# Performance work log

Measured on AMD Instinct MI355X. Metric: run time of the kernel, lower is better.

The kernel has to match this reference:

```python
import jax, jax.numpy as jnp
import numpy as np

B, T, D = 4, 2048, 1024
H = 16
DH = D // H
BASE = 10000.0


def _rope_tables(seq_len, dim):
    inv_freq = 1.0 / (BASE ** (np.arange(0, dim, 2, dtype=np.float32) / dim))
    pos = np.arange(seq_len, dtype=np.float32)
    freqs = np.outer(pos, inv_freq)            # (T, dim/2)
    emb = np.concatenate([freqs, freqs], -1)   # (T, dim)
    return jnp.asarray(np.cos(emb)), jnp.asarray(np.sin(emb))


def setup_inputs() -> dict:
    key = jax.random.key(0)
    ks = jax.random.split(key, 5)
    s = 1.0 / np.sqrt(D)
    x = jax.random.normal(ks[0], (B, T, D), jnp.float32)
    Wqkv = jax.random.normal(ks[1], (D, 3 * D), jnp.float32) * s
    bqkv = jnp.zeros((3 * D,), jnp.float32)
    Wproj = jax.random.normal(ks[2], (D, D), jnp.float32) * s
    bproj = jnp.zeros((D,), jnp.float32)
    cos, sin = _rope_tables(T, DH)
    return {"x": x, "Wqkv": Wqkv, "bqkv": bqkv, "Wproj": Wproj,
            "bproj": bproj, "cos": cos, "sin": sin}


def _rotate_half(u):
    u1, u2 = jnp.split(u, 2, axis=-1)
    return jnp.concatenate([-u2, u1], axis=-1)


def reference(x, Wqkv, bqkv, Wproj, bproj, cos, sin):
    b, t, d = x.shape
    qkv = x @ Wqkv + bqkv                       # (B, T, 3D)
    qkv = qkv.reshape(b, t, 3, H, DH)           # matches '(three h d)' order
    q, k, v = qkv[:, :, 0], qkv[:, :, 1], qkv[:, :, 2]  # (B, T, H, DH)
    c = cos[None, :, None, :]                   # (1, T, 1, DH)
    s = sin[None, :, None, :]
    q = q * c + _rotate_half(q) * s
    k = k * c + _rotate_half(k) * s
    scale = DH ** -0.5
    attn = jnp.einsum('bthd,bshd->bhts', q, k) * scale   # (B, H, T, T)
    attn = jax.nn.softmax(attn, axis=-1)
    out = jnp.einsum('bhts,bshd->bthd', attn, v)          # (B, T, H, DH)
    out = out.reshape(b, t, d)
    return out @ Wproj + bproj
```

## Files before the change

### kernel.cpp

```cpp
#include <hip/hip_runtime.h>


typedef _Float16 half_t;
typedef _Float16 half8 __attribute__((ext_vector_type(8)));
typedef _Float16 half4v __attribute__((ext_vector_type(4)));
typedef float floatx4 __attribute__((ext_vector_type(4)));

#define MFMA_F16 __builtin_amdgcn_mfma_f32_16x16x32_f16

constexpr int Bdim = 4, T = 2048, D = 1024, H = 16, DH = 64;
constexpr int Mrows = Bdim * T;
constexpr int N1 = 3 * D;
constexpr int KD = D;

constexpr float QSCALE = 0.125f * 1.4426950408889634f;
constexpr float CSHIFT = 4.0f * 1.4426950408889634f;

__global__ __launch_bounds__(256) void cvt_kernel(const float* __restrict__ s,
                                                  half_t* __restrict__ d, int n4) {
  int i = blockIdx.x * 256 + threadIdx.x;
  if (i < n4) {
    float4 v = ((const float4*)s)[i];
    half4v h;
    h[0] = (half_t)v.x; h[1] = (half_t)v.y; h[2] = (half_t)v.z; h[3] = (half_t)v.w;
    ((half4v*)d)[i] = h;
  }
}

__global__ __launch_bounds__(64) void cvt_transpose(const float* __restrict__ W,
                                                    half_t* __restrict__ Wt,
                                                    int Kr, int Nc) {
  __shared__ half_t Th[32][36];
  const int l = threadIdx.x;
  const int n0 = blockIdx.x * 32, k0 = blockIdx.y * 32;
#pragma unroll
  for (int i = 0; i < 4; ++i) {
    int kk = (l >> 3) + i * 8;
    int nn4 = (l & 7) * 4;
    float4 v = *(const float4*)(W + (size_t)(k0 + kk) * Nc + n0 + nn4);
    half4v h;
    h[0] = (half_t)v.x; h[1] = (half_t)v.y; h[2] = (half_t)v.z; h[3] = (half_t)v.w;
    *(half4v*)&Th[kk][nn4] = h;
  }
  __syncthreads();
#pragma unroll
  for (int i = 0; i < 4; ++i) {
    int nn = (l >> 3) + i * 8;
    int kk4 = (l & 7) * 4;
    half4v h;
#pragma unroll
    for (int j = 0; j < 4; ++j) h[j] = Th[kk4 + j][nn];
    *(half4v*)(Wt + (size_t)(n0 + nn) * Kr + k0 + kk4) = h;
  }
}

__global__ __launch_bounds__(256) void gemm_qkv_rope(
    const half_t* __restrict__ X, const half_t* __restrict__ Wt,
    const float* __restrict__ bias, const float* __restrict__ cosT,
    const float* __restrict__ sinT,
    half_t* __restrict__ Q, half_t* __restrict__ K, half_t* __restrict__ V) {
  __shared__ half_t As[128][40];
  __shared__ half_t Bs[128][40];
  const int tid = threadIdx.x;
  const int lane = tid & 63, wv = tid >> 6;
  const int wm = wv >> 1, wn = wv & 1;
  const int qd = lane >> 4, ln = lane & 15;
  const int bn = blockIdx.x, bm = blockIdx.y;

  floatx4 acc[4][4] = {};

  for (int k0 = 0; k0 < KD; k0 += 32) {
#pragma unroll
    for (int p = 0; p < 2; ++p) {
      int c = tid + p * 256;
      int row = c >> 2, col = (c & 3) << 3;
      *(half8*)&As[row][col] =
          *(const half8*)(X + (size_t)(bm * 128 + row) * KD + k0 + col);
      *(half8*)&Bs[row][col] =
          *(const half8*)(Wt + (size_t)(bn * 128 + row) * KD + k0 + col);
    }
    __syncthreads();

    half8 af[4], bf[4];
#pragma unroll
    for (int mi = 0; mi < 4; ++mi)
      af[mi] = *(const half8*)&As[wm * 64 + mi * 16 + ln][qd * 8];
#pragma unroll
    for (int ni = 0; ni < 4; ++ni)
      bf[ni] = *(const half8*)&Bs[wn * 64 + ni * 16 + ln][qd * 8];
#pragma unroll
    for (int mi = 0; mi < 4; ++mi)
#pragma unroll
      for (int ni = 0; ni < 4; ++ni)
        acc[mi][ni] = MFMA_F16(af[mi], bf[ni], acc[mi][ni], 0, 0, 0);
    __syncthreads();
  }

  const int n0 = bn * 128 + wn * 64;
  const int sreg = n0 >> 10;
  const int h = (n0 & 1023) >> 6;
  half_t* OUT = (sreg == 0) ? Q : (sreg == 1) ? K : V;
  const float qscale = (sreg == 0) ? QSCALE : 1.0f;
  float bv[4];
#pragma unroll
  for (int ni = 0; ni < 4; ++ni) bv[ni] = bias[n0 + ni * 16 + ln];

#pragma unroll
  for (int mi = 0; mi < 4; ++mi) {
#pragma unroll
    for (int r = 0; r < 4; ++r) {
      int m = bm * 128 + wm * 64 + mi * 16 + qd * 4 + r;
      int b = m >> 11, t = m & (T - 1);
      float v0 = acc[mi][0][r] + bv[0];
      float v1 = acc[mi][1][r] + bv[1];
      float v2 = acc[mi][2][r] + bv[2];
      float v3 = acc[mi][3][r] + bv[3];
      float o0, o1, o2, o3;
      if (sreg < 2) {
        float c0 = cosT[t * 64 + ln],      s0 = sinT[t * 64 + ln];
        float c1 = cosT[t * 64 + 16 + ln], s1 = sinT[t * 64 + 16 + ln];
        float c2 = cosT[t * 64 + 32 + ln], s2 = sinT[t * 64 + 32 + ln];
        float c3 = cosT[t * 64 + 48 + ln], s3 = sinT[t * 64 + 48 + ln];
        o0 = v0 * c0 - v2 * s0;
        o1 = v1 * c1 - v3 * s1;
        o2 = v2 * c2 + v0 * s2;
        o3 = v3 * c3 + v1 * s3;
      } else {
        o0 = v0; o1 = v1; o2 = v2; o3 = v3;
      }
      size_t base = ((size_t)(b * H + h) * T + t) * DH;
      OUT[base + 0 * 16 + ln] = (half_t)(o0 * qscale);
      OUT[base + 1 * 16 + ln] = (half_t)(o1 * qscale);
      OUT[base + 2 * 16 + ln] = (half_t)(o2 * qscale);
      OUT[base + 3 * 16 + ln] = (half_t)(o3 * qscale);
    }
  }
}

__global__ __launch_bounds__(256, 4) void flash_attn(
    const half_t* __restrict__ Q, const half_t* __restrict__ K,
    const half_t* __restrict__ V, half_t* __restrict__ AO) {
  __shared__ half_t Klds[64][72];
  __shared__ half_t Vt[64][72];
  __shared__ half_t Plds[4][32][72];
  const int tid = threadIdx.x;
  const int lane = tid & 63, wv = tid >> 6;
  const int qd = lane >> 4, ln = lane & 15;
  const int bh = blockIdx.y;
  const int q0 = blockIdx.x * 128 + wv * 32;
  const half_t* Qb = Q + (size_t)bh * T * DH;
  const half_t* Kb = K + (size_t)bh * T * DH;
  const half_t* Vb = V + (size_t)bh * T * DH;

  half8 qf[2][2];
#pragma unroll
  for (int mi = 0; mi < 2; ++mi)
#pragma unroll
    for (int ks = 0; ks < 2; ++ks)
      qf[mi][ks] = *(const half8*)(Qb + (size_t)(q0 + mi * 16 + ln) * DH + ks * 32 + qd * 8);

  floatx4 Oacc[2][4] = {};
  floatx4 Lacc[2] = {};
  half8 ones;
#pragma unroll
  for (int j = 0; j < 8; ++j) ones[j] = (half_t)1.0f;

  const int pswz = (ln >> 2) & 3;

  for (int s0 = 0; s0 < T; s0 += 64) {
#pragma unroll
    for (int p = 0; p < 2; ++p) {
      int c = tid + p * 256;
      int s = c & 63, dh0 = (c >> 6) << 3;
      *(half8*)&Klds[s][dh0] = *(const half8*)(Kb + (size_t)(s0 + s) * DH + dh0);
      half8 vv = *(const half8*)(Vb + (size_t)(s0 + s) * DH + dh0);
#pragma unroll
      for (int i = 0; i < 8; ++i) Vt[dh0 + i][s] = vv[i];
    }
    __syncthreads();

    floatx4 sacc[2][4] = {};
#pragma unroll
    for (int ks = 0; ks < 2; ++ks)
#pragma unroll
      for (int ni = 0; ni < 4; ++ni) {
        half8 kf = *(const half8*)&Klds[ni * 16 + ln][ks * 32 + qd * 8];
#pragma unroll
        for (int mi = 0; mi < 2; ++mi)
          sacc[mi][ni] = MFMA_F16(qf[mi][ks], kf, sacc[mi][ni], 0, 0, 0);
      }

#pragma unroll
    for (int mi = 0; mi < 2; ++mi)
#pragma unroll
      for (int ni = 0; ni < 4; ++ni) {
        int colw = ((((ni * 2) + (ln >> 3)) ^ qd) << 3) | (ln & 7);
#pragma unroll
        for (int r = 0; r < 4; ++r) {
          float p = __builtin_amdgcn_exp2f(sacc[mi][ni][r] - CSHIFT);
          Plds[wv][mi * 16 + qd * 4 + r][colw] = (half_t)p;
        }
      }

#pragma unroll
    for (int ks = 0; ks < 2; ++ks) {
      half8 pf[2];
#pragma unroll
      for (int mi = 0; mi < 2; ++mi)
        pf[mi] = *(const half8*)&Plds[wv][mi * 16 + ln][((ks * 4 + qd) ^ pswz) << 3];
#pragma unroll
      for (int ni = 0; ni < 4; ++ni) {
        half8 vf = *(const half8*)&Vt[ni * 16 + ln][ks * 32 + qd * 8];
#pragma unroll
        for (int mi = 0; mi < 2; ++mi)
          Oacc[mi][ni] = MFMA_F16(pf[mi], vf, Oacc[mi][ni], 0, 0, 0);
      }
#pragma unroll
      for (int mi = 0; mi < 2; ++mi)
        Lacc[mi] = MFMA_F16(pf[mi], ones, Lacc[mi], 0, 0, 0);
    }
    __syncthreads();
  }

  const int b = bh >> 4, h = bh & 15;
#pragma unroll
  for (int mi = 0; mi < 2; ++mi) {
#pragma unroll
    for (int r = 0; r < 4; ++r) {
      float invL = 1.f / Lacc[mi][r];
      int t = q0 + mi * 16 + qd * 4 + r;
      size_t base = ((size_t)b * T + t) * D + h * DH;
#pragma unroll
      for (int ni = 0; ni < 4; ++ni)
        AO[base + ni * 16 + ln] = (half_t)(Oacc[mi][ni][r] * invL);
    }
  }
}

__global__ __launch_bounds__(256) void gemm_proj(
    const half_t* __restrict__ X, const half_t* __restrict__ Wt,
    const float* __restrict__ bias, float* __restrict__ OUTF) {
  __shared__ half_t As[128][40];
  __shared__ half_t Bs[128][40];
  const int tid = threadIdx.x;
  const int lane = tid & 63, wv = tid >> 6;
  const int wm = wv >> 1, wn = wv & 1;
  const int qd = lane >> 4, ln = lane & 15;
  const int bn = blockIdx.x, bm = blockIdx.y;

  floatx4 acc[4][4] = {};

  for (int k0 = 0; k0 < KD; k0 += 32) {
#pragma unroll
    for (int p = 0; p < 2; ++p) {
      int c = tid + p * 256;
      int row = c >> 2, col = (c & 3) << 3;
      *(half8*)&As[row][col] =
          *(const half8*)(X + (size_t)(bm * 128 + row) * KD + k0 + col);
      *(half8*)&Bs[row][col] =
          *(const half8*)(Wt + (size_t)(bn * 128 + row) * KD + k0 + col);
    }
    __syncthreads();

    half8 af[4], bf[4];
#pragma unroll
    for (int mi = 0; mi < 4; ++mi)
      af[mi] = *(const half8*)&As[wm * 64 + mi * 16 + ln][qd * 8];
#pragma unroll
    for (int ni = 0; ni < 4; ++ni)
      bf[ni] = *(const half8*)&Bs[wn * 64 + ni * 16 + ln][qd * 8];
#pragma unroll
    for (int mi = 0; mi < 4; ++mi)
#pragma unroll
      for (int ni = 0; ni < 4; ++ni)
        acc[mi][ni] = MFMA_F16(af[mi], bf[ni], acc[mi][ni], 0, 0, 0);
    __syncthreads();
  }

  const int n0 = bn * 128 + wn * 64;
  float bv[4];
#pragma unroll
  for (int ni = 0; ni < 4; ++ni) bv[ni] = bias[n0 + ni * 16 + ln];
#pragma unroll
  for (int mi = 0; mi < 4; ++mi) {
#pragma unroll
    for (int r = 0; r < 4; ++r) {
      int m = bm * 128 + wm * 64 + mi * 16 + qd * 4 + r;
#pragma unroll
      for (int ni = 0; ni < 4; ++ni)
        OUTF[(size_t)m * D + n0 + ni * 16 + ln] = acc[mi][ni][r] + bv[ni];
    }
  }
}

extern "C" void kernel_launch(void* const* d_in, const int* in_sizes, int n_in,
                              void* d_out, int out_size, void* d_ws, size_t ws_size,
                              hipStream_t stream) {
  const float* x     = (const float*)d_in[0];
  const float* Wqkv  = (const float*)d_in[1];
  const float* bqkv  = (const float*)d_in[2];
  const float* Wproj = (const float*)d_in[3];
  const float* bproj = (const float*)d_in[4];
  const float* cosT  = (const float*)d_in[5];
  const float* sinT  = (const float*)d_in[6];
  float* out = (float*)d_out;

  half_t* xh      = (half_t*)d_ws;
  half_t* Wqkvt   = xh + (size_t)Mrows * KD;
  half_t* Wprojt  = Wqkvt + (size_t)KD * N1;
  half_t* Qb      = Wprojt + (size_t)D * D;
  half_t* Kb      = Qb + (size_t)Bdim * H * T * DH;
  half_t* Vb      = Kb + (size_t)Bdim * H * T * DH;
  half_t* AO      = xh;

  cvt_kernel<<<(Mrows * KD / 4 + 255) / 256, 256, 0, stream>>>(x, xh, Mrows * KD / 4);
  cvt_transpose<<<dim3(N1 / 32, KD / 32), 64, 0, stream>>>(Wqkv, Wqkvt, KD, N1);
  cvt_transpose<<<dim3(D / 32, KD / 32), 64, 0, stream>>>(Wproj, Wprojt, KD, D);

  gemm_qkv_rope<<<dim3(N1 / 128, Mrows / 128), 256, 0, stream>>>(
      xh, Wqkvt, bqkv, cosT, sinT, Qb, Kb, Vb);
  flash_attn<<<dim3(T / 128, Bdim * H), 256, 0, stream>>>(Qb, Kb, Vb, AO);
  gemm_proj<<<dim3(D / 128, Mrows / 128), 256, 0, stream>>>(AO, Wprojt, bproj, out);
}
```

Measured before the change: 332.5 us.

## Transpose V in QKV epilogue, keep P in registers, use direct global-to-LDS loads

The QKV GEMM epilogue now writes V pre-transposed (head-dim major), so the attention kernel no longer does a scalar LDS transpose of V. Attention computes S^T via swapped MFMA operands so probabilities stay in registers and feed 16x16x16 MFMAs directly, which removes the P round-trip through LDS and the ones-MFMA row sum. Row sums are now accumulated in registers and reduced with shuffles. Both GEMMs switch to global_load_lds direct loads into unpadded LDS tiles, which drops the register staging but may add bank conflicts on the fragment reads. The occupancy hint of 4 on the attention kernel is also removed.

```diff
diff --git a/kernel.cpp b/kernel.cpp
--- a/kernel.cpp
+++ b/kernel.cpp
@@ -7,6 +7,7 @@
 typedef float floatx4 __attribute__((ext_vector_type(4)));
 
 #define MFMA_F16 __builtin_amdgcn_mfma_f32_16x16x32_f16
+#define MFMA16   __builtin_amdgcn_mfma_f32_16x16x16f16
 
 constexpr int Bdim = 4, T = 2048, D = 1024, H = 16, DH = 64;
 constexpr int Mrows = Bdim * T;
@@ -15,6 +16,12 @@
 
 constexpr float QSCALE = 0.125f * 1.4426950408889634f;
 constexpr float CSHIFT = 4.0f * 1.4426950408889634f;
+
+__device__ __forceinline__ void gl_lds16(const half_t* g, half_t* l) {
+  __builtin_amdgcn_global_load_lds(
+      (const __attribute__((address_space(1))) void*)g,
+      (__attribute__((address_space(3))) void*)l, 16, 0, 0);
+}
 
 __global__ __launch_bounds__(256) void cvt_kernel(const float* __restrict__ s,
                                                   half_t* __restrict__ d, int n4) {
@@ -59,8 +66,8 @@
     const float* __restrict__ bias, const float* __restrict__ cosT,
     const float* __restrict__ sinT,
     half_t* __restrict__ Q, half_t* __restrict__ K, half_t* __restrict__ V) {
-  __shared__ half_t As[128][40];
-  __shared__ half_t Bs[128][40];
+  __shared__ half_t As[128 * 32];
+  __shared__ half_t Bs[128 * 32];
   const int tid = threadIdx.x;
   const int lane = tid & 63, wv = tid >> 6;
   const int wm = wv >> 1, wn = wv & 1;
@@ -74,20 +81,18 @@
     for (int p = 0; p < 2; ++p) {
       int c = tid + p * 256;
       int row = c >> 2, col = (c & 3) << 3;
-      *(half8*)&As[row][col] =
-          *(const half8*)(X + (size_t)(bm * 128 + row) * KD + k0 + col);
-      *(half8*)&Bs[row][col] =
-          *(const half8*)(Wt + (size_t)(bn * 128 + row) * KD + k0 + col);
+      gl_lds16(X + (size_t)(bm * 128 + row) * KD + k0 + col, As + c * 8);
+      gl_lds16(Wt + (size_t)(bn * 128 + row) * KD + k0 + col, Bs + c * 8);
     }
     __syncthreads();
 
     half8 af[4], bf[4];
 #pragma unroll
     for (int mi = 0; mi < 4; ++mi)
-      af[mi] = *(const half8*)&As[wm * 64 + mi * 16 + ln][qd * 8];
+      af[mi] = *(const half8*)&As[(wm * 64 + mi * 16 + ln) * 32 + qd * 8];
 #pragma unroll
     for (int ni = 0; ni < 4; ++ni)
-      bf[ni] = *(const half8*)&Bs[wn * 64 + ni * 16 + ln][qd * 8];
+      bf[ni] = *(const half8*)&Bs[(wn * 64 + ni * 16 + ln) * 32 + qd * 8];
 #pragma unroll
     for (int mi = 0; mi < 4; ++mi)
 #pragma unroll
@@ -99,50 +104,60 @@
   const int n0 = bn * 128 + wn * 64;
   const int sreg = n0 >> 10;
   const int h = (n0 & 1023) >> 6;
-  half_t* OUT = (sreg == 0) ? Q : (sreg == 1) ? K : V;
-  const float qscale = (sreg == 0) ? QSCALE : 1.0f;
   float bv[4];
 #pragma unroll
   for (int ni = 0; ni < 4; ++ni) bv[ni] = bias[n0 + ni * 16 + ln];
 
-#pragma unroll
-  for (int mi = 0; mi < 4; ++mi) {
-#pragma unroll
-    for (int r = 0; r < 4; ++r) {
-      int m = bm * 128 + wm * 64 + mi * 16 + qd * 4 + r;
-      int b = m >> 11, t = m & (T - 1);
-      float v0 = acc[mi][0][r] + bv[0];
-      float v1 = acc[mi][1][r] + bv[1];
-      float v2 = acc[mi][2][r] + bv[2];
-      float v3 = acc[mi][3][r] + bv[3];
-      float o0, o1, o2, o3;
-      if (sreg < 2) {
+  if (sreg == 2) {
+#pragma unroll
+    for (int mi = 0; mi < 4; ++mi) {
+      int m0 = bm * 128 + wm * 64 + mi * 16 + qd * 4;
+      int b = m0 >> 11, t0 = m0 & (T - 1);
+#pragma unroll
+      for (int ni = 0; ni < 4; ++ni) {
+        int dh = ni * 16 + ln;
+        half4v hv;
+#pragma unroll
+        for (int r = 0; r < 4; ++r) hv[r] = (half_t)(acc[mi][ni][r] + bv[ni]);
+        *(half4v*)(V + ((size_t)(b * H + h) * DH + dh) * T + t0) = hv;
+      }
+    }
+  } else {
+    const float qscale = (sreg == 0) ? QSCALE : 1.0f;
+    half_t* OUT = (sreg == 0) ? Q : K;
+#pragma unroll
+    for (int mi = 0; mi < 4; ++mi) {
+#pragma unroll
+      for (int r = 0; r < 4; ++r) {
+        int m = bm * 128 + wm * 64 + mi * 16 + qd * 4 + r;
+        int b = m >> 11, t = m & (T - 1);
+        float v0 = acc[mi][0][r] + bv[0];
+        float v1 = acc[mi][1][r] + bv[1];
+        float v2 = acc[mi][2][r] + bv[2];
+        float v3 = acc[mi][3][r] + bv[3];
         float c0 = cosT[t * 64 + ln],      s0 = sinT[t * 64 + ln];
         float c1 = cosT[t * 64 + 16 + ln], s1 = sinT[t * 64 + 16 + ln];
         float c2 = cosT[t * 64 + 32 + ln], s2 = sinT[t * 64 + 32 + ln];
         float c3 = cosT[t * 64 + 48 + ln], s3 = sinT[t * 64 + 48 + ln];
-        o0 = v0 * c0 - v2 * s0;
-        o1 = v1 * c1 - v3 * s1;
-        o2 = v2 * c2 + v0 * s2;
-        o3 = v3 * c3 + v1 * s3;
-      } else {
-        o0 = v0; o1 = v1; o2 = v2; o3 = v3;
-      }
-      size_t base = ((size_t)(b * H + h) * T + t) * DH;
-      OUT[base + 0 * 16 + ln] = (half_t)(o0 * qscale);
-      OUT[base + 1 * 16 + ln] = (half_t)(o1 * qscale);
-      OUT[base + 2 * 16 + ln] = (half_t)(o2 * qscale);
-      OUT[base + 3 * 16 + ln] = (half_t)(o3 * qscale);
-    }
-  }
-}
-
-__global__ __launch_bounds__(256, 4) void flash_attn(
+        float o0 = v0 * c0 - v2 * s0;
+        float o1 = v1 * c1 - v3 * s1;
+        float o2 = v2 * c2 + v0 * s2;
+        float o3 = v3 * c3 + v1 * s3;
+        size_t base = ((size_t)(b * H + h) * T + t) * DH;
+        OUT[base + 0 * 16 + ln] = (half_t)(o0 * qscale);
+        OUT[base + 1 * 16 + ln] = (half_t)(o1 * qscale);
+        OUT[base + 2 * 16 + ln] = (half_t)(o2 * qscale);
+        OUT[base + 3 * 16 + ln] = (half_t)(o3 * qscale);
+      }
+    }
+  }
+}
+
+__global__ __launch_bounds__(256) void flash_attn(
     const half_t* __restrict__ Q, const half_t* __restrict__ K,
-    const half_t* __restrict__ V, half_t* __restrict__ AO) {
+    const half_t* __restrict__ Vt, half_t* __restrict__ AO) {
   __shared__ half_t Klds[64][72];
-  __shared__ half_t Vt[64][72];
-  __shared__ half_t Plds[4][32][72];
+  __shared__ half_t Vlds[64][72];
   const int tid = threadIdx.x;
   const int lane = tid & 63, wv = tid >> 6;
   const int qd = lane >> 4, ln = lane & 15;
@@ -150,7 +165,7 @@
   const int q0 = blockIdx.x * 128 + wv * 32;
   const half_t* Qb = Q + (size_t)bh * T * DH;
   const half_t* Kb = K + (size_t)bh * T * DH;
-  const half_t* Vb = V + (size_t)bh * T * DH;
+  const half_t* Vb = Vt + (size_t)bh * DH * T;
 
   half8 qf[2][2];
 #pragma unroll
@@ -160,26 +175,19 @@
       qf[mi][ks] = *(const half8*)(Qb + (size_t)(q0 + mi * 16 + ln) * DH + ks * 32 + qd * 8);
 
   floatx4 Oacc[2][4] = {};
-  floatx4 Lacc[2] = {};
-  half8 ones;
-#pragma unroll
-  for (int j = 0; j < 8; ++j) ones[j] = (half_t)1.0f;
-
-  const int pswz = (ln >> 2) & 3;
+  float Ls[2] = {0.f, 0.f};
 
   for (int s0 = 0; s0 < T; s0 += 64) {
 #pragma unroll
     for (int p = 0; p < 2; ++p) {
-      int c = tid + p * 256;
-      int s = c & 63, dh0 = (c >> 6) << 3;
-      *(half8*)&Klds[s][dh0] = *(const half8*)(Kb + (size_t)(s0 + s) * DH + dh0);
-      half8 vv = *(const half8*)(Vb + (size_t)(s0 + s) * DH + dh0);
-#pragma unroll
-      for (int i = 0; i < 8; ++i) Vt[dh0 + i][s] = vv[i];
-    }
-    __syncthreads();
-
-    floatx4 sacc[2][4] = {};
+      int idx = tid + p * 256;
+      int r = idx >> 3, ch = (idx & 7) << 3;
+      *(half8*)&Klds[r][ch] = *(const half8*)(Kb + (size_t)(s0 + r) * DH + ch);
+      *(half8*)&Vlds[r][ch] = *(const half8*)(Vb + (size_t)r * T + s0 + ch);
+    }
+    __syncthreads();
+
+    floatx4 sacc[4][2] = {};
 #pragma unroll
     for (int ks = 0; ks < 2; ++ks)
 #pragma unroll
@@ -187,39 +195,39 @@
         half8 kf = *(const half8*)&Klds[ni * 16 + ln][ks * 32 + qd * 8];
 #pragma unroll
         for (int mi = 0; mi < 2; ++mi)
-          sacc[mi][ni] = MFMA_F16(qf[mi][ks], kf, sacc[mi][ni], 0, 0, 0);
-      }
-
-#pragma unroll
-    for (int mi = 0; mi < 2; ++mi)
-#pragma unroll
-      for (int ni = 0; ni < 4; ++ni) {
-        int colw = ((((ni * 2) + (ln >> 3)) ^ qd) << 3) | (ln & 7);
-#pragma unroll
-        for (int r = 0; r < 4; ++r) {
-          float p = __builtin_amdgcn_exp2f(sacc[mi][ni][r] - CSHIFT);
-          Plds[wv][mi * 16 + qd * 4 + r][colw] = (half_t)p;
-        }
-      }
-
-#pragma unroll
-    for (int ks = 0; ks < 2; ++ks) {
-      half8 pf[2];
-#pragma unroll
-      for (int mi = 0; mi < 2; ++mi)
-        pf[mi] = *(const half8*)&Plds[wv][mi * 16 + ln][((ks * 4 + qd) ^ pswz) << 3];
-#pragma unroll
-      for (int ni = 0; ni < 4; ++ni) {
-        half8 vf = *(const half8*)&Vt[ni * 16 + ln][ks * 32 + qd * 8];
+          sacc[ni][mi] = MFMA_F16(kf, qf[mi][ks], sacc[ni][mi], 0, 0, 0);
+      }
+
+    half4v pf[2][4];
+#pragma unroll
+    for (int ni = 0; ni < 4; ++ni)
+#pragma unroll
+      for (int mi = 0; mi < 2; ++mi) {
+        float p0 = __builtin_amdgcn_exp2f(sacc[ni][mi][0] - CSHIFT);
+        float p1 = __builtin_amdgcn_exp2f(sacc[ni][mi][1] - CSHIFT);
+        float p2 = __builtin_amdgcn_exp2f(sacc[ni][mi][2] - CSHIFT);
+        float p3 = __builtin_amdgcn_exp2f(sacc[ni][mi][3] - CSHIFT);
+        Ls[mi] += (p0 + p1) + (p2 + p3);
+        half4v h; h[0] = (half_t)p0; h[1] = (half_t)p1; h[2] = (half_t)p2; h[3] = (half_t)p3;
+        pf[mi][ni] = h;
+      }
+
+#pragma unroll
+    for (int ni = 0; ni < 4; ++ni)
+#pragma unroll
+      for (int di = 0; di < 4; ++di) {
+        half4v vf = *(const half4v*)&Vlds[di * 16 + ln][ni * 16 + qd * 4];
 #pragma unroll
         for (int mi = 0; mi < 2; ++mi)
-          Oacc[mi][ni] = MFMA_F16(pf[mi], vf, Oacc[mi][ni], 0, 0, 0);
-      }
-#pragma unroll
-      for (int mi = 0; mi < 2; ++mi)
-        Lacc[mi] = MFMA_F16(pf[mi], ones, Lacc[mi], 0, 0, 0);
-    }
-    __syncthreads();
+          Oacc[mi][di] = MFMA16(pf[mi][ni], vf, Oacc[mi][di], 0, 0, 0);
+      }
+    __syncthreads();
+  }
+
+#pragma unroll
+  for (int mi = 0; mi < 2; ++mi) {
+    Ls[mi] += __shfl_xor(Ls[mi], 16);
+    Ls[mi] += __shfl_xor(Ls[mi], 32);
   }
 
   const int b = bh >> 4, h = bh & 15;
@@ -227,12 +235,12 @@
   for (int mi = 0; mi < 2; ++mi) {
 #pragma unroll
     for (int r = 0; r < 4; ++r) {
-      float invL = 1.f / Lacc[mi][r];
+      float invL = 1.f / __shfl(Ls[mi], qd * 4 + r);
       int t = q0 + mi * 16 + qd * 4 + r;
       size_t base = ((size_t)b * T + t) * D + h * DH;
 #pragma unroll
-      for (int ni = 0; ni < 4; ++ni)
-        AO[base + ni * 16 + ln] = (half_t)(Oacc[mi][ni][r] * invL);
+      for (int di = 0; di < 4; ++di)
+        AO[base + di * 16 + ln] = (half_t)(Oacc[mi][di][r] * invL);
     }
   }
 }
@@ -240,8 +248,8 @@
 __global__ __launch_bounds__(256) void gemm_proj(
     const half_t* __restrict__ X, const half_t* __restrict__ Wt,
     const float* __restrict__ bias, float* __restrict__ OUTF) {
-  __shared__ half_t As[128][40];
-  __shared__ half_t Bs[128][40];
+  __shared__ half_t As[128 * 32];
+  __shared__ half_t Bs[128 * 32];
   const int tid = threadIdx.x;
   const int lane = tid & 63, wv = tid >> 6;
   const int wm = wv >> 1, wn = wv & 1;
@@ -255,20 +263,18 @@
     for (int p = 0; p < 2; ++p) {
       int c = tid + p * 256;
       int row = c >> 2, col = (c & 3) << 3;
-      *(half8*)&As[row][col] =
-          *(const half8*)(X + (size_t)(bm * 128 + row) * KD + k0 + col);
-      *(half8*)&Bs[row][col] =
-          *(const half8*)(Wt + (size_t)(bn * 128 + row) * KD + k0 + col);
+      gl_lds16(X + (size_t)(bm * 128 + row) * KD + k0 + col, As + c * 8);
+      gl_lds16(Wt + (size_t)(bn * 128 + row) * KD + k0 + col, Bs + c * 8);
     }
     __syncthreads();
 
     half8 af[4], bf[4];
 #pragma unroll
     for (int mi = 0; mi < 4; ++mi)
-      af[mi] = *(const half8*)&As[wm * 64 + mi * 16 + ln][qd * 8];
+      af[mi] = *(const half8*)&As[(wm * 64 + mi * 16 + ln) * 32 + qd * 8];
 #pragma unroll
     for (int ni = 0; ni < 4; ++ni)
-      bf[ni] = *(const half8*)&Bs[wn * 64 + ni * 16 + ln][qd * 8];
+      bf[ni] = *(const half8*)&Bs[(wn * 64 + ni * 16 + ln) * 32 + qd * 8];
 #pragma unroll
     for (int mi = 0; mi < 4; ++mi)
 #pragma unroll
```

After: 361.9 us. 1.09x slower.
